# Optimization experiments

Measured on AMD Instinct MI355X. Metric: run time of the kernel, lower is better.

Reference implementation:

```python
import jax, jax.numpy as jnp
import numpy as np

KY, KX = 3, 3  # kernel_size from init_kwargs


def setup_inputs() -> dict:
    key = jax.random.key(0)
    x = jax.random.normal(key, (8, 32, 512, 512), dtype=jnp.float32)
    return {"x": x}


def reference(x):
    # Replicate-pad H by (KY-1)//2, W by (KX-1)//2 (matches F.pad mode='replicate').
    py, px = (KY - 1) // 2, (KX - 1) // 2
    B, C, H, W = x.shape
    padded = jnp.pad(x, ((0, 0), (0, 0), (py, py), (px, px)), mode='edge')
    center = (KY * KX) // 2
    # The torch module builds an identity neigh2channel kernel with the center
    # tap zeroed, then maxes over the KY*KX channels. The zeroed center channel
    # contributes a constant 0 to that max, so we initialize the running max at 0
    # and fold in every non-center neighbor via shifted slices (no blown-up
    # [B,C,KY*KX,H,W] tensor is materialized).
    m = jnp.zeros_like(x)
    for idx in range(KY * KX):
        if idx == center:
            continue
        i, j = divmod(idx, KX)
        m = jnp.maximum(m, padded[:, :, i:i + H, j:j + W])
    mask = (x > m).astype(x.dtype)
    return x * mask
```

## Files before the change

kernel.cpp:

```cpp
#include <hip/hip_runtime.h>


#define IMG_W 512
#define IMG_H 512
#define NPLANES 256
#define CHUNK 32
#define THREADS 256
#define WAVES_PER_BLOCK (THREADS / 64)
#define CHUNKS_PER_PLANE (IMG_H / CHUNK)

typedef float v4f __attribute__((ext_vector_type(4)));

static_assert(IMG_W == 64 * 8, "one wave covers a full row at 8 floats/lane");
static_assert(IMG_H % CHUNK == 0, "chunks divide evenly");

__device__ __forceinline__ void load_row(const float* __restrict__ base, int r,
                                         float (&d)[8]) {
    const v4f a = *(const v4f*)(base + (size_t)r * IMG_W);
    const v4f b = *(const v4f*)(base + (size_t)r * IMG_W + 4);
    d[0] = a.x; d[1] = a.y; d[2] = a.z; d[3] = a.w;
    d[4] = b.x; d[5] = b.y; d[6] = b.z; d[7] = b.w;
}

__device__ __forceinline__ void row_stats(const float (&d)[8], int lane,
                                          float (&lr)[8], float (&hm)[8]) {
    float lnb = __shfl_up(d[7], 1);
    lnb = (lane == 0) ? d[0] : lnb;
    float rnb = __shfl_down(d[0], 1);
    rnb = (lane == 63) ? d[7] : rnb;

    lr[0] = fmaxf(lnb,  d[1]);
    lr[1] = fmaxf(d[0], d[2]);
    lr[2] = fmaxf(d[1], d[3]);
    lr[3] = fmaxf(d[2], d[4]);
    lr[4] = fmaxf(d[3], d[5]);
    lr[5] = fmaxf(d[4], d[6]);
    lr[6] = fmaxf(d[5], d[7]);
    lr[7] = fmaxf(d[6], rnb);
#pragma unroll
    for (int i = 0; i < 8; ++i) hm[i] = fmaxf(lr[i], d[i]);
}

__global__ __launch_bounds__(THREADS, 4)
void nms3x3_kernel(const float* __restrict__ x, float* __restrict__ out) {
    const int wid   = blockIdx.x * WAVES_PER_BLOCK + (threadIdx.x >> 6);
    const int lane  = threadIdx.x & 63;
    const int plane = wid / CHUNKS_PER_PLANE;
    const int chunk = wid % CHUNKS_PER_PLANE;
    const int r0    = chunk * CHUNK;

    const float* img  = x   + (size_t)plane * IMG_H * IMG_W + lane * 8;
    float*       oimg = out + (size_t)plane * IMG_H * IMG_W + lane * 8;

    float pd[8], cd[8], nd[8];
    float pHm[8], cLr[8], cHm[8], nLr[8], nHm[8];
    float junk[8];

    load_row(img, (r0 > 0) ? r0 - 1 : 0, pd);
    row_stats(pd, lane, junk, pHm);
    load_row(img, r0, cd);
    row_stats(cd, lane, cLr, cHm);

#pragma unroll 4
    for (int k = 0; k < CHUNK; ++k) {
        const int r  = r0 + k;
        const int rn = (r + 1 < IMG_H) ? r + 1 : IMG_H - 1;
        load_row(img, rn, nd);
        row_stats(nd, lane, nLr, nHm);

        float o[8];
#pragma unroll
        for (int i = 0; i < 8; ++i) {
            float m = fmaxf(fmaxf(pHm[i], nHm[i]), cLr[i]);
            m = fmaxf(m, 0.0f);
            o[i] = (cd[i] > m) ? cd[i] : 0.0f;
        }

        *(v4f*)(oimg + (size_t)r * IMG_W)     = (v4f){ o[0], o[1], o[2], o[3] };
        *(v4f*)(oimg + (size_t)r * IMG_W + 4) = (v4f){ o[4], o[5], o[6], o[7] };

#pragma unroll
        for (int i = 0; i < 8; ++i) {
            pHm[i] = cHm[i];
            cd[i]  = nd[i];
            cLr[i] = nLr[i];
            cHm[i] = nHm[i];
        }
    }
}

extern "C" void kernel_launch(void* const* d_in, const int* in_sizes, int n_in,
                              void* d_out, int out_size, void* d_ws, size_t ws_size,
                              hipStream_t stream) {
    const float* x = (const float*)d_in[0];
    float* out     = (float*)d_out;
    const int total_waves = NPLANES * CHUNKS_PER_PLANE;
    dim3 grid(total_waves / WAVES_PER_BLOCK);
    nms3x3_kernel<<<grid, dim3(THREADS), 0, stream>>>(x, out);
}
```

Measured before the change: 444.8 us.

## Shrink row chunks to 8 and issue all row loads upfront per wave

Reduces rows per wave from 32 to 8, quadrupling the number of waves, and fully unrolls the chunk so all ten input rows are loaded before any compute. This raises memory-level parallelism and occupancy to better hide HBM latency on a bandwidth-bound stencil. In exchange, halo reads rise from 34/32 to 10/8 per output row, register use grows, and the launch-bounds occupancy hint is dropped.

New measurement: 437.9 us. No clear change (-1.5%).

```diff
diff --git a/kernel.cpp b/kernel.cpp
--- a/kernel.cpp
+++ b/kernel.cpp
@@ -4,7 +4,7 @@
 #define IMG_W 512
 #define IMG_H 512
 #define NPLANES 256
-#define CHUNK 32
+#define CHUNK 8
 #define THREADS 256
 #define WAVES_PER_BLOCK (THREADS / 64)
 #define CHUNKS_PER_PLANE (IMG_H / CHUNK)
@@ -41,52 +41,67 @@
     for (int i = 0; i < 8; ++i) hm[i] = fmaxf(lr[i], d[i]);
 }
 
-__global__ __launch_bounds__(THREADS, 4)
+__global__ __launch_bounds__(THREADS)
 void nms3x3_kernel(const float* __restrict__ x, float* __restrict__ out) {
     const int wid   = blockIdx.x * WAVES_PER_BLOCK + (threadIdx.x >> 6);
     const int lane  = threadIdx.x & 63;
-    const int plane = wid / CHUNKS_PER_PLANE;
-    const int chunk = wid % CHUNKS_PER_PLANE;
+    const int plane = wid >> 6;
+    const int chunk = wid & 63;
     const int r0    = chunk * CHUNK;
 
     const float* img  = x   + (size_t)plane * IMG_H * IMG_W + lane * 8;
     float*       oimg = out + (size_t)plane * IMG_H * IMG_W + lane * 8;
 
-    float pd[8], cd[8], nd[8];
-    float pHm[8], cLr[8], cHm[8], nLr[8], nHm[8];
-    float junk[8];
+    float d0[8], d1[8], d2[8], d3[8], d4[8], d5[8], d6[8], d7[8], d8[8], d9[8];
+    const int rT = (r0 > 0) ? r0 - 1 : 0;
+    const int rB = (r0 + CHUNK < IMG_H) ? r0 + CHUNK : IMG_H - 1;
+    load_row(img, rT,     d0);
+    load_row(img, r0 + 0, d1);
+    load_row(img, r0 + 1, d2);
+    load_row(img, r0 + 2, d3);
+    load_row(img, r0 + 3, d4);
+    load_row(img, r0 + 4, d5);
+    load_row(img, r0 + 5, d6);
+    load_row(img, r0 + 6, d7);
+    load_row(img, r0 + 7, d8);
+    load_row(img, rB,     d9);
 
-    load_row(img, (r0 > 0) ? r0 - 1 : 0, pd);
-    row_stats(pd, lane, junk, pHm);
-    load_row(img, r0, cd);
-    row_stats(cd, lane, cLr, cHm);
+    float hmP[8], hmC[8], lrC[8], junk[8];
+    row_stats(d0, lane, junk, hmP);
+    row_stats(d1, lane, lrC, hmC);
 
-#pragma unroll 4
-    for (int k = 0; k < CHUNK; ++k) {
-        const int r  = r0 + k;
-        const int rn = (r + 1 < IMG_H) ? r + 1 : IMG_H - 1;
-        load_row(img, rn, nd);
-        row_stats(nd, lane, nLr, nHm);
+#define ROW_STEP(K, DC, DN)                                                    \
+    {                                                                          \
+        float lrN[8], hmN[8];                                                  \
+        row_stats(DN, lane, lrN, hmN);                                         \
+        float o[8];                                                            \
+        _Pragma("unroll")                                                      \
+        for (int i = 0; i < 8; ++i) {                                          \
+            float m = fmaxf(fmaxf(hmP[i], hmN[i]), lrC[i]);                    \
+            m = fmaxf(m, 0.0f);                                                \
+            o[i] = (DC[i] > m) ? DC[i] : 0.0f;                                 \
+        }                                                                      \
+        *(v4f*)(oimg + (size_t)(r0 + K) * IMG_W)                               \
+            = (v4f){ o[0], o[1], o[2], o[3] };                                 \
+        *(v4f*)(oimg + (size_t)(r0 + K) * IMG_W + 4)                           \
+            = (v4f){ o[4], o[5], o[6], o[7] };                                 \
+        _Pragma("unroll")                                                      \
+        for (int i = 0; i < 8; ++i) {                                          \
+            hmP[i] = hmC[i];                                                   \
+            hmC[i] = hmN[i];                                                   \
+            lrC[i] = lrN[i];                                                   \
+        }                                                                      \
+    }
 
-        float o[8];
-#pragma unroll
-        for (int i = 0; i < 8; ++i) {
-            float m = fmaxf(fmaxf(pHm[i], nHm[i]), cLr[i]);
-            m = fmaxf(m, 0.0f);
-            o[i] = (cd[i] > m) ? cd[i] : 0.0f;
-        }
-
-        *(v4f*)(oimg + (size_t)r * IMG_W)     = (v4f){ o[0], o[1], o[2], o[3] };
-        *(v4f*)(oimg + (size_t)r * IMG_W + 4) = (v4f){ o[4], o[5], o[6], o[7] };
-
-#pragma unroll
-        for (int i = 0; i < 8; ++i) {
-            pHm[i] = cHm[i];
-            cd[i]  = nd[i];
-            cLr[i] = nLr[i];
-            cHm[i] = nHm[i];
-        }
-    }
+    ROW_STEP(0, d1, d2)
+    ROW_STEP(1, d2, d3)
+    ROW_STEP(2, d3, d4)
+    ROW_STEP(3, d4, d5)
+    ROW_STEP(4, d5, d6)
+    ROW_STEP(5, d6, d7)
+    ROW_STEP(6, d7, d8)
+    ROW_STEP(7, d8, d9)
+#undef ROW_STEP
 }
 
 extern "C" void kernel_launch(void* const* d_in, const int* in_sizes, int n_in,
```
